# Optimization experiments

Hardware: AMD Instinct MI355X
Metric: run time of the kernel (lower is better)

The kernel has to match this reference:

```python
import jax, jax.numpy as jnp
import numpy as np

HORIZON = 60
HID = 128

def setup_inputs() -> dict:
    key = jax.random.key(0)
    ks = jax.random.split(key, 7)
    B, D, O = 16384, 256, 3
    s_ih = 1.0 / np.sqrt(HID)
    return {
        "x": jax.random.normal(ks[0], (B, D), jnp.float32),
        "W_ih": jax.random.normal(ks[1], (3 * HID, D), jnp.float32) * s_ih,
        "W_hh": jax.random.normal(ks[2], (3 * HID, HID), jnp.float32) * s_ih,
        "b_ih": jax.random.normal(ks[3], (3 * HID,), jnp.float32) * s_ih,
        "b_hh": jax.random.normal(ks[4], (3 * HID,), jnp.float32) * s_ih,
        "W_out": jax.random.normal(ks[5], (O, HID), jnp.float32) * s_ih,
        "b_out": jax.random.normal(ks[6], (O,), jnp.float32) * s_ih,
    }

def reference(x, W_ih, W_hh, b_ih, b_hh, W_out, b_out):
    # Input is identical at every timestep -> precompute input projection once.
    B = x.shape[0]
    gi = x @ W_ih.T + b_ih                      # [B, 3H]
    gi_r, gi_z, gi_n = jnp.split(gi, 3, axis=-1)

    def step(h, _):
        gh = h @ W_hh.T + b_hh                  # [B, 3H]
        gh_r, gh_z, gh_n = jnp.split(gh, 3, axis=-1)
        r = jax.nn.sigmoid(gi_r + gh_r)
        z = jax.nn.sigmoid(gi_z + gh_z)
        n = jnp.tanh(gi_n + r * gh_n)
        h_new = (1.0 - z) * n + z * h           # torch GRU update
        return h_new, h_new

    h0 = jnp.zeros((B, HID), x.dtype)
    _, hs = jax.lax.scan(step, h0, None, length=HORIZON)   # [T, B, H]
    out = jnp.einsum('tbh,oh->bto', hs, W_out) + b_out     # [B, T, O]
    return out
```

## Files before the change

### kernel.cpp

```cpp
#include <hip/hip_runtime.h>


typedef __attribute__((ext_vector_type(8))) short short8;
typedef __attribute__((ext_vector_type(4))) float f32x4;

#define MFMA16(a, b, c) __builtin_amdgcn_mfma_f32_16x16x32_bf16((a), (b), (c), 0, 0, 0)

__device__ __forceinline__ short f2bf(float x) {
    union { float f; unsigned u; } v; v.f = x;
    unsigned r = v.u + 0x7FFFu + ((v.u >> 16) & 1u);
    return (short)(r >> 16);
}

__device__ __forceinline__ unsigned cvtpk(float lo, float hi) {
    unsigned d;
    asm("v_cvt_pk_bf16_f32 %0, %1, %2" : "=v"(d) : "v"(lo), "v"(hi));
    return d;
}

__device__ __forceinline__ short8 cvt8(const float* __restrict__ p) {
    f32x4 a = *(const f32x4*)p;
    f32x4 b = *(const f32x4*)(p + 4);
    short8 r;
    r[0] = f2bf(a[0]); r[1] = f2bf(a[1]); r[2] = f2bf(a[2]); r[3] = f2bf(a[3]);
    r[4] = f2bf(b[0]); r[5] = f2bf(b[1]); r[6] = f2bf(b[2]); r[7] = f2bf(b[3]);
    return r;
}
__device__ __forceinline__ short8 cvt8s(const float* __restrict__ p, float s) {
    f32x4 a = *(const f32x4*)p;
    f32x4 b = *(const f32x4*)(p + 4);
    short8 r;
    r[0] = f2bf(a[0] * s); r[1] = f2bf(a[1] * s); r[2] = f2bf(a[2] * s); r[3] = f2bf(a[3] * s);
    r[4] = f2bf(b[0] * s); r[5] = f2bf(b[1] * s); r[6] = f2bf(b[2] * s); r[7] = f2bf(b[3] * s);
    return r;
}

__global__ __launch_bounds__(512, 2) void gru_traj_kernel(
    const float* __restrict__ x,
    const float* __restrict__ W_ih,
    const float* __restrict__ W_hh,
    const float* __restrict__ b_ih,
    const float* __restrict__ b_hh,
    const float* __restrict__ W_out,
    const float* __restrict__ b_out,
    float* __restrict__ out)
{
    const int tid  = threadIdx.x;
    const int wid  = tid >> 6;
    const int lane = tid & 63;
    const int l15  = lane & 15;
    const int l4   = lane >> 4;
    const int b0   = blockIdx.x << 6;
    const int hb   = wid << 4;

    const float SCL  = -1.442695041f;
    const float SCL2 = -2.885390082f;

    __shared__ short hbuf[2][64 * 128];
    __shared__ short wobuf[3 * 136];

    {
        int* z = (int*)hbuf[0];
        #pragma unroll
        for (int i = 0; i < 8; ++i) z[tid + i * 512] = 0;
    }
    if (tid < 384) wobuf[(tid >> 7) * 136 + (tid & 127)] = f2bf(W_out[tid]);

    short8 wfrag[3][4];
    #pragma unroll
    for (int kt = 0; kt < 4; ++kt) {
        wfrag[0][kt] = cvt8s(W_hh + (size_t)(      hb + l15) * 128 + kt * 32 + l4 * 8, SCL);
        wfrag[1][kt] = cvt8s(W_hh + (size_t)(128 + hb + l15) * 128 + kt * 32 + l4 * 8, SCL);
        wfrag[2][kt] = cvt8 (W_hh + (size_t)(256 + hb + l15) * 128 + kt * 32 + l4 * 8);
    }

    const int bbase = hb + l4 * 4;
    const f32x4 bR4 = (*(const f32x4*)(b_ih + bbase)       + *(const f32x4*)(b_hh + bbase))       * SCL;
    const f32x4 bZ4 = (*(const f32x4*)(b_ih + 128 + bbase) + *(const f32x4*)(b_hh + 128 + bbase)) * SCL;
    const f32x4 bNi = *(const f32x4*)(b_ih + 256 + bbase);
    const f32x4 bNh = *(const f32x4*)(b_hh + 256 + bbase);
    const float bo0 = b_out[0], bo1 = b_out[1], bo2 = b_out[2];

    f32x4 initR[4], initZ[4], giN[4];
    #pragma unroll
    for (int q = 0; q < 4; ++q) { initR[q] = bR4; initZ[q] = bZ4; giN[q] = bNi; }
    #pragma unroll
    for (int kt = 0; kt < 8; ++kt) {
        short8 a0 = cvt8s(W_ih + (size_t)(      hb + l15) * 256 + kt * 32 + l4 * 8, SCL);
        short8 a1 = cvt8s(W_ih + (size_t)(128 + hb + l15) * 256 + kt * 32 + l4 * 8, SCL);
        short8 a2 = cvt8 (W_ih + (size_t)(256 + hb + l15) * 256 + kt * 32 + l4 * 8);
        #pragma unroll
        for (int q = 0; q < 4; ++q) {
            short8 bx = cvt8(x + (size_t)(b0 + q * 16 + l15) * 256 + kt * 32 + l4 * 8);
            initR[q] = MFMA16(a0, bx, initR[q]);
            initZ[q] = MFMA16(a1, bx, initZ[q]);
            giN [q] = MFMA16(a2, bx, giN [q]);
        }
    }

    float hq[4][4];
    #pragma unroll
    for (int q = 0; q < 4; ++q)
        #pragma unroll
        for (int r = 0; r < 4; ++r) hq[q][r] = 0.f;

    const int s8 = (wid << 2) | l4;
    int roff[4];
    #pragma unroll
    for (int kt = 0; kt < 4; ++kt)
        roff[kt] = (l15 * 128 + (((kt * 4 + l4) ^ l15) & 15) * 8) * 2;
    const int woff = (l15 * 128 + (((s8 >> 1) ^ l15) & 15) * 8 + (s8 & 1) * 4) * 2;

    __syncthreads();

    #pragma unroll 2
    for (int t = 0; t < 60; ++t) {
        const char* rb = (const char*)hbuf[t & 1];
        char*       wb = (char*)hbuf[(t & 1) ^ 1];

        short8 afc[4], afn[4];
        #pragma unroll
        for (int kt = 0; kt < 4; ++kt)
            afc[kt] = *(const short8*)(rb + roff[kt]);

        #pragma unroll
        for (int q = 0; q < 4; ++q) {
            if (q < 3) {
                #pragma unroll
                for (int kt = 0; kt < 4; ++kt)
                    afn[kt] = *(const short8*)(rb + roff[kt] + (q + 1) * 4096);
            }

            f32x4 aR = initR[q], aZ = initZ[q], aN = bNh;
            #pragma unroll
            for (int kt = 0; kt < 4; ++kt) {
                aR = MFMA16(wfrag[0][kt], afc[kt], aR);
                aZ = MFMA16(wfrag[1][kt], afc[kt], aZ);
                aN = MFMA16(wfrag[2][kt], afc[kt], aN);
            }

            if (t > 0 && wid == ((q + t) & 7)) {
                f32x4 oa = (f32x4){0.f, 0.f, 0.f, 0.f};
                #pragma unroll
                for (int kt = 0; kt < 4; ++kt) {
                    short8 wo = {0, 0, 0, 0, 0, 0, 0, 0};
                    if (l15 < 3) wo = *(const short8*)(wobuf + l15 * 136 + kt * 32 + l4 * 8);
                    oa = MFMA16(wo, afc[kt], oa);
                }
                if (l4 == 0) {
                    float* op = out + (size_t)(b0 + q * 16 + l15) * 180 + (t - 1) * 3;
                    op[0] = oa[0] + bo0; op[1] = oa[1] + bo1; op[2] = oa[2] + bo2;
                }
            }

            float hn[4];
            #pragma unroll
            for (int r = 0; r < 4; ++r) {
                float eA = __builtin_amdgcn_exp2f(aR[r]);
                float eB = __builtin_amdgcn_exp2f(aZ[r]);
                float A  = 1.0f + eA, Bv = 1.0f + eB;
                float R  = __builtin_amdgcn_rcpf(A * Bv);
                float rr = R * Bv;
                float zz = R * A;
                float sn = fmaf(rr, aN[r], giN[q][r]);
                float eC = __builtin_amdgcn_exp2f(sn * SCL2);
                float nn = fmaf(2.0f, __builtin_amdgcn_rcpf(1.0f + eC), -1.0f);
                hn[r] = fmaf(zz, hq[q][r] - nn, nn);
                hq[q][r] = hn[r];
            }
            uint2 pk;
            pk.x = cvtpk(hn[0], hn[1]);
            pk.y = cvtpk(hn[2], hn[3]);
            *(uint2*)(wb + woff + q * 4096) = pk;

            #pragma unroll
            for (int kt = 0; kt < 4; ++kt) afc[kt] = afn[kt];
        }
        __syncthreads();
    }

    if (wid < 4) {
        const int q = wid;
        const char* rb = (const char*)hbuf[0];
        f32x4 oa = (f32x4){0.f, 0.f, 0.f, 0.f};
        #pragma unroll
        for (int kt = 0; kt < 4; ++kt) {
            short8 af = *(const short8*)(rb + roff[kt] + q * 4096);
            short8 wo = {0, 0, 0, 0, 0, 0, 0, 0};
            if (l15 < 3) wo = *(const short8*)(wobuf + l15 * 136 + kt * 32 + l4 * 8);
            oa = MFMA16(wo, af, oa);
        }
        if (l4 == 0) {
            float* op = out + (size_t)(b0 + q * 16 + l15) * 180 + 59 * 3;
            op[0] = oa[0] + bo0; op[1] = oa[1] + bo1; op[2] = oa[2] + bo2;
        }
    }
}

extern "C" void kernel_launch(void* const* d_in, const int* in_sizes, int n_in,
                              void* d_out, int out_size, void* d_ws, size_t ws_size,
                              hipStream_t stream) {
    const float* x     = (const float*)d_in[0];
    const float* W_ih  = (const float*)d_in[1];
    const float* W_hh  = (const float*)d_in[2];
    const float* b_ih  = (const float*)d_in[3];
    const float* b_hh  = (const float*)d_in[4];
    const float* W_out = (const float*)d_in[5];
    const float* b_out = (const float*)d_in[6];
    float* out = (float*)d_out;

    const int B = in_sizes[0] / 256;
    hipLaunchKernelGGL(gru_traj_kernel, dim3(B / 64), dim3(512), 0, stream,
                       x, W_ih, W_hh, b_ih, b_hh, W_out, b_out, out);
}
```

Baseline: 154.4 us.

## Hold W_out fragments in registers and double-buffer per-quarter LDS loads

Converts W_out into bf16 MFMA fragments held in registers once, replacing the LDS wobuf and its per-timestep reloads in the output projection. The per-quarter hidden-state loads are rewritten as an explicit two-buffer ping-pong (afA/afB) so the next quarter's LDS reads are issued before the current quarter's MFMAs. The gate math is also rewritten as 4-wide vector expressions. This raises register pressure under the 512-thread, 2-block launch bounds, which could cause spills or lower occupancy.

```diff
diff --git a/kernel.cpp b/kernel.cpp
--- a/kernel.cpp
+++ b/kernel.cpp
@@ -57,14 +57,12 @@
     const float SCL2 = -2.885390082f;
 
     __shared__ short hbuf[2][64 * 128];
-    __shared__ short wobuf[3 * 136];
 
     {
         int* z = (int*)hbuf[0];
         #pragma unroll
         for (int i = 0; i < 8; ++i) z[tid + i * 512] = 0;
     }
-    if (tid < 384) wobuf[(tid >> 7) * 136 + (tid & 127)] = f2bf(W_out[tid]);
 
     short8 wfrag[3][4];
     #pragma unroll
@@ -72,6 +70,13 @@
         wfrag[0][kt] = cvt8s(W_hh + (size_t)(      hb + l15) * 128 + kt * 32 + l4 * 8, SCL);
         wfrag[1][kt] = cvt8s(W_hh + (size_t)(128 + hb + l15) * 128 + kt * 32 + l4 * 8, SCL);
         wfrag[2][kt] = cvt8 (W_hh + (size_t)(256 + hb + l15) * 128 + kt * 32 + l4 * 8);
+    }
+    short8 wofrag[4];
+    #pragma unroll
+    for (int kt = 0; kt < 4; ++kt) {
+        short8 f = {0, 0, 0, 0, 0, 0, 0, 0};
+        if (l15 < 3) f = cvt8(W_out + l15 * 128 + kt * 32 + l4 * 8);
+        wofrag[kt] = f;
     }
 
     const int bbase = hb + l4 * 4;
@@ -98,11 +103,9 @@
         }
     }
 
-    float hq[4][4];
-    #pragma unroll
-    for (int q = 0; q < 4; ++q)
-        #pragma unroll
-        for (int r = 0; r < 4; ++r) hq[q][r] = 0.f;
+    f32x4 hq[4];
+    #pragma unroll
+    for (int q = 0; q < 4; ++q) hq[q] = (f32x4){0.f, 0.f, 0.f, 0.f};
 
     const int s8 = (wid << 2) | l4;
     int roff[4];
@@ -112,70 +115,78 @@
     const int woff = (l15 * 128 + (((s8 >> 1) ^ l15) & 15) * 8 + (s8 & 1) * 4) * 2;
 
     __syncthreads();
+
+#define LOADQ(buf, q)                                             \
+    {                                                             \
+        _Pragma("unroll")                                         \
+        for (int kt = 0; kt < 4; ++kt)                            \
+            buf[kt] = *(const short8*)(rb + roff[kt] + (q) * 4096); \
+    }
+
+#define PROCQ(q, AF)                                                          \
+    {                                                                         \
+        f32x4 aR = initR[q], aZ = initZ[q], aN = bNh;                         \
+        _Pragma("unroll")                                                     \
+        for (int kt = 0; kt < 4; ++kt) {                                      \
+            aR = MFMA16(wfrag[0][kt], AF[kt], aR);                            \
+            aZ = MFMA16(wfrag[1][kt], AF[kt], aZ);                            \
+            aN = MFMA16(wfrag[2][kt], AF[kt], aN);                            \
+        }                                                                     \
+        if (t > 0 && wid == (((q) + t) & 7)) {                                \
+            f32x4 oa = (f32x4){0.f, 0.f, 0.f, 0.f};                           \
+            _Pragma("unroll")                                                 \
+            for (int kt = 0; kt < 4; ++kt) oa = MFMA16(wofrag[kt], AF[kt], oa); \
+            if (l4 == 0) {                                                    \
+                float* op = out + (size_t)(b0 + (q) * 16 + l15) * 180 + (t - 1) * 3; \
+                op[0] = oa[0] + bo0; op[1] = oa[1] + bo1; op[2] = oa[2] + bo2; \
+            }                                                                 \
+        }                                                                     \
+        f32x4 eA, eB;                                                         \
+        _Pragma("unroll")                                                     \
+        for (int r = 0; r < 4; ++r) {                                         \
+            eA[r] = __builtin_amdgcn_exp2f(aR[r]);                            \
+            eB[r] = __builtin_amdgcn_exp2f(aZ[r]);                            \
+        }                                                                     \
+        f32x4 A  = eA + 1.0f;                                                 \
+        f32x4 Bv = eB + 1.0f;                                                 \
+        f32x4 P  = A * Bv;                                                    \
+        f32x4 R;                                                              \
+        _Pragma("unroll")                                                     \
+        for (int r = 0; r < 4; ++r) R[r] = __builtin_amdgcn_rcpf(P[r]);       \
+        f32x4 rr = R * Bv;                                                    \
+        f32x4 zz = R * A;                                                     \
+        f32x4 sn = rr * aN + giN[q];                                          \
+        f32x4 eC;                                                             \
+        _Pragma("unroll")                                                     \
+        for (int r = 0; r < 4; ++r) eC[r] = __builtin_amdgcn_exp2f(sn[r] * SCL2); \
+        f32x4 C1 = eC + 1.0f;                                                 \
+        f32x4 T;                                                              \
+        _Pragma("unroll")                                                     \
+        for (int r = 0; r < 4; ++r) T[r] = __builtin_amdgcn_rcpf(C1[r]);      \
+        f32x4 nn = 2.0f * T - 1.0f;                                           \
+        f32x4 hn = (hq[q] - nn) * zz + nn;                                    \
+        hq[q] = hn;                                                           \
+        uint2 pk;                                                             \
+        pk.x = cvtpk(hn[0], hn[1]);                                           \
+        pk.y = cvtpk(hn[2], hn[3]);                                           \
+        *(uint2*)(wb + woff + (q) * 4096) = pk;                               \
+    }
 
     #pragma unroll 2
     for (int t = 0; t < 60; ++t) {
         const char* rb = (const char*)hbuf[t & 1];
         char*       wb = (char*)hbuf[(t & 1) ^ 1];
 
-        short8 afc[4], afn[4];
-        #pragma unroll
-        for (int kt = 0; kt < 4; ++kt)
-            afc[kt] = *(const short8*)(rb + roff[kt]);
-
-        #pragma unroll
-        for (int q = 0; q < 4; ++q) {
-            if (q < 3) {
-                #pragma unroll
-                for (int kt = 0; kt < 4; ++kt)
-                    afn[kt] = *(const short8*)(rb + roff[kt] + (q + 1) * 4096);
-            }
-
-            f32x4 aR = initR[q], aZ = initZ[q], aN = bNh;
-            #pragma unroll
-            for (int kt = 0; kt < 4; ++kt) {
-                aR = MFMA16(wfrag[0][kt], afc[kt], aR);
-                aZ = MFMA16(wfrag[1][kt], afc[kt], aZ);
-                aN = MFMA16(wfrag[2][kt], afc[kt], aN);
-            }
-
-            if (t > 0 && wid == ((q + t) & 7)) {
-                f32x4 oa = (f32x4){0.f, 0.f, 0.f, 0.f};
-                #pragma unroll
-                for (int kt = 0; kt < 4; ++kt) {
-                    short8 wo = {0, 0, 0, 0, 0, 0, 0, 0};
-                    if (l15 < 3) wo = *(const short8*)(wobuf + l15 * 136 + kt * 32 + l4 * 8);
-                    oa = MFMA16(wo, afc[kt], oa);
-                }
-                if (l4 == 0) {
-                    float* op = out + (size_t)(b0 + q * 16 + l15) * 180 + (t - 1) * 3;
-                    op[0] = oa[0] + bo0; op[1] = oa[1] + bo1; op[2] = oa[2] + bo2;
-                }
-            }
-
-            float hn[4];
-            #pragma unroll
-            for (int r = 0; r < 4; ++r) {
-                float eA = __builtin_amdgcn_exp2f(aR[r]);
-                float eB = __builtin_amdgcn_exp2f(aZ[r]);
-                float A  = 1.0f + eA, Bv = 1.0f + eB;
-                float R  = __builtin_amdgcn_rcpf(A * Bv);
-                float rr = R * Bv;
-                float zz = R * A;
-                float sn = fmaf(rr, aN[r], giN[q][r]);
-                float eC = __builtin_amdgcn_exp2f(sn * SCL2);
-                float nn = fmaf(2.0f, __builtin_amdgcn_rcpf(1.0f + eC), -1.0f);
-                hn[r] = fmaf(zz, hq[q][r] - nn, nn);
-                hq[q][r] = hn[r];
-            }
-            uint2 pk;
-            pk.x = cvtpk(hn[0], hn[1]);
-            pk.y = cvtpk(hn[2], hn[3]);
-            *(uint2*)(wb + woff + q * 4096) = pk;
-
-            #pragma unroll
-            for (int kt = 0; kt < 4; ++kt) afc[kt] = afn[kt];
-        }
+        short8 afA[4], afB[4];
+        LOADQ(afA, 0);
+        LOADQ(afB, 1);
+        PROCQ(0, afA);
+        LOADQ(afA, 2);
+        PROCQ(1, afB);
+        LOADQ(afB, 3);
+        PROCQ(2, afA);
+        PROCQ(3, afB);
+
         __syncthreads();
     }
 
@@ -186,15 +197,15 @@
         #pragma unroll
         for (int kt = 0; kt < 4; ++kt) {
             short8 af = *(const short8*)(rb + roff[kt] + q * 4096);
-            short8 wo = {0, 0, 0, 0, 0, 0, 0, 0};
-            if (l15 < 3) wo = *(const short8*)(wobuf + l15 * 136 + kt * 32 + l4 * 8);
-            oa = MFMA16(wo, af, oa);
+            oa = MFMA16(wofrag[kt], af, oa);
         }
         if (l4 == 0) {
             float* op = out + (size_t)(b0 + q * 16 + l15) * 180 + 59 * 3;
             op[0] = oa[0] + bo0; op[1] = oa[1] + bo1; op[2] = oa[2] + bo2;
         }
     }
+#undef LOADQ
+#undef PROCQ
 }
 
 extern "C" void kernel_launch(void* const* d_in, const int* in_sizes, int n_in,
```

New measurement: 149.7 us. 3.0% less time.
